# Kernel optimization log

Hardware: AMD Instinct MI355X
Metric: run time of the kernel (lower is better)

## Reference

```python
import jax, jax.numpy as jnp
import numpy as np

SHIFT_MIN, SHIFT_MAX = -14.0, 0.0  # deepshift range for weight_bits=5: (-(2**4-2), 0)


def shift_quant(w):
    """Quantize weights to signed powers of two (bit-shift weights), STE form."""
    sign = jnp.sign(w)
    shift = jnp.clip(jnp.round(jnp.log2(jnp.abs(w) + 1e-12)), SHIFT_MIN, SHIFT_MAX)
    q = sign * jnp.exp2(shift)
    return w + jax.lax.stop_gradient(q - w)


def moe_fc(t, wg, w0, b0, w1, b1):
    """Top-1 routing over 2 experts: expert0 dense Linear, expert1 shift-quantized Linear.
    t: [T, C]; weights torch-layout [out, in]. With top_k=1 the softmaxed top-k gate is 1.0,
    so combine is a hard select of the chosen expert's output."""
    logits = t @ wg                      # [T, 2]
    pick0 = (jnp.argmax(logits, axis=-1) == 0)[:, None]
    y0 = t @ w0.T + b0                   # dense expert
    y1 = t @ shift_quant(w1).T + b1      # shift expert
    return jnp.where(pick0, y0, y1)


def setup_inputs() -> dict:
    key = jax.random.key(0)
    ks = jax.random.split(key, 10)
    B, N, C, Dh = 16, 1024, 512, 2048
    s = 0.02
    return {
        "x": jax.random.normal(ks[0], (B, N, C), jnp.float32),
        "H": 32,
        "W": 32,
        "wg1": jax.random.normal(ks[1], (C, 2), jnp.float32) * s,
        "fc1_w0": jax.random.normal(ks[2], (Dh, C), jnp.float32) * s,
        "fc1_b0": jnp.zeros((Dh,), jnp.float32),
        "fc1_w1": jax.random.normal(ks[3], (Dh, C), jnp.float32) * s,
        "fc1_b1": jnp.zeros((Dh,), jnp.float32),
        "dw_w": jax.random.normal(ks[4], (Dh, 1, 3, 3), jnp.float32) * np.sqrt(2.0 / 9.0),
        "dw_b": jnp.zeros((Dh,), jnp.float32),
        "wg2": jax.random.normal(ks[5], (Dh, 2), jnp.float32) * s,
        "fc2_w0": jax.random.normal(ks[6], (C, Dh), jnp.float32) * s,
        "fc2_b0": jnp.zeros((C,), jnp.float32),
        "fc2_w1": jax.random.normal(ks[7], (C, Dh), jnp.float32) * s,
        "fc2_b1": jnp.zeros((C,), jnp.float32),
    }


def reference(x, H, W, wg1, fc1_w0, fc1_b0, fc1_w1, fc1_b1, dw_w, dw_b,
              wg2, fc2_w0, fc2_b0, fc2_w1, fc2_b1):
    B, N, C = x.shape
    Dh = fc1_w0.shape[0]
    # fc1 MoE
    h = moe_fc(x.reshape(-1, C), wg1, fc1_w0, fc1_b0, fc1_w1, fc1_b1)  # [B*N, Dh]
    # DWConv 3x3 depthwise, NCHW
    h = h.reshape(B, N, Dh).transpose(0, 2, 1).reshape(B, Dh, H, W)
    h = jax.lax.conv_general_dilated(
        h, dw_w, window_strides=(1, 1), padding="SAME",
        dimension_numbers=("NCHW", "OIHW", "NCHW"), feature_group_count=Dh)
    h = h + dw_b[None, :, None, None]
    h = h.reshape(B, Dh, N).transpose(0, 2, 1)  # [B, N, Dh]
    # GELU (exact, as nn.GELU default); dropout p=0 -> identity
    h = jax.nn.gelu(h, approximate=False)
    # fc2 MoE
    y = moe_fc(h.reshape(-1, Dh), wg2, fc2_w0, fc2_b0, fc2_w1, fc2_b1)
    return y.reshape(B, N, -1)
```

## Files before the change

### kernel.cpp

```cpp
#include <hip/hip_runtime.h>
#include <hip/hip_bf16.h>


#define TOKS  16384
#define CIN   512
#define DHID  2048

typedef __attribute__((ext_vector_type(8))) __bf16 bf16x8;
typedef __attribute__((ext_vector_type(4))) float  f32x4;
typedef __attribute__((ext_vector_type(4))) float  float4v;
typedef __attribute__((ext_vector_type(4))) unsigned short ushort4v;

__device__ __forceinline__ unsigned short f2bf(float f) {
  union { float f; unsigned int u; } a; a.f = f;
  unsigned int u = a.u;
  unsigned int r = u + 0x7FFFu + ((u >> 16) & 1u);
  return (unsigned short)(r >> 16);
}
__device__ __forceinline__ float bf2f(unsigned short h) {
  union { unsigned int u; float f; } a; a.u = ((unsigned int)h) << 16;
  return a.f;
}

__device__ __forceinline__ float squant(float w) {
  if (w == 0.0f) return 0.0f;
  float aw = fabsf(w) + 1e-12f;
  union { float f; unsigned u; } a; a.f = aw;
  int e = (int)((a.u >> 23) & 0xFFu) - 127;
  unsigned frac = a.u & 0x7FFFFFu;
  int shift = e + (frac >= 0x3504F4u ? 1 : 0);
  shift = min(max(shift, -14), 0);
  union { unsigned u; float f; } q; q.u = (unsigned)(shift + 127) << 23;
  return (w > 0.0f) ? q.f : -q.f;
}

#define GLDS16(gp, lp) __builtin_amdgcn_global_load_lds(                      \
    (const __attribute__((address_space(1))) void*)(gp),                      \
    (__attribute__((address_space(3))) void*)(lp), 16, 0, 0)

__global__ void k_prep(const float* __restrict__ w0, const float* __restrict__ w1,
                       const float* __restrict__ w20, const float* __restrict__ w21,
                       unsigned short* __restrict__ w0hi, unsigned short* __restrict__ w0lo,
                       unsigned short* __restrict__ w1q, unsigned short* __restrict__ w20b,
                       unsigned short* __restrict__ w21b) {
  int i = blockIdx.x * 256 + threadIdx.x;
  if (i >= DHID * CIN) return;
  float v = w0[i];
  unsigned short h = f2bf(v);
  w0hi[i] = h;
  w0lo[i] = f2bf(v - bf2f(h));
  w1q[i]  = f2bf(squant(w1[i]));
  w20b[i] = f2bf(w20[i]);
  w21b[i] = f2bf(squant(w21[i]));
}

__global__ void k_prepx(const float* __restrict__ x,
                        unsigned short* __restrict__ xhi, unsigned short* __restrict__ xlo) {
  int i = blockIdx.x * 256 + threadIdx.x;
  float4v v = ((const float4v*)x)[i];
  ushort4v hv, lv;
  #pragma unroll
  for (int q = 0; q < 4; ++q) {
    unsigned short h = f2bf(v[q]);
    hv[q] = h;
    lv[q] = f2bf(v[q] - bf2f(h));
  }
  ((ushort4v*)xhi)[i] = hv;
  ((ushort4v*)xlo)[i] = lv;
}

__global__ void k_gate1(const float* __restrict__ x, const float* __restrict__ wg1,
                        unsigned char* __restrict__ pick1) {
  int tok = blockIdx.x * 4 + (threadIdx.x >> 6);
  int l = threadIdx.x & 63;
  const float* xr = x + (size_t)tok * CIN;
  float s0 = 0.f, s1 = 0.f;
  for (int i = l; i < CIN; i += 64) {
    float v = xr[i];
    s0 += v * wg1[i * 2 + 0];
    s1 += v * wg1[i * 2 + 1];
  }
  for (int m = 32; m; m >>= 1) { s0 += __shfl_xor(s0, m); s1 += __shfl_xor(s1, m); }
  if (l == 0) pick1[tok] = (s0 >= s1) ? 0 : 1;
}

__global__ void k_scan(const unsigned char* __restrict__ pick, int* __restrict__ perm,
                       int* __restrict__ n0buf) {
  __shared__ int cnt[1024];
  const int t = threadIdx.x;
  unsigned char loc[16];
  int c0 = 0;
  #pragma unroll
  for (int i = 0; i < 16; ++i) { loc[i] = pick[t * 16 + i]; c0 += (loc[i] == 0); }
  cnt[t] = c0;
  __syncthreads();
  for (int off = 1; off < 1024; off <<= 1) {
    int v = cnt[t] + ((t >= off) ? cnt[t - off] : 0);
    __syncthreads();
    cnt[t] = v;
    __syncthreads();
  }
  int total0 = cnt[1023];
  int pre0 = cnt[t] - c0;
  int pre1 = t * 16 - pre0;
  if (t == 0) n0buf[0] = total0;
  int p0 = pre0, p1 = total0 + pre1;
  #pragma unroll
  for (int i = 0; i < 16; ++i) {
    int tok = t * 16 + i;
    if (loc[i] == 0) perm[p0++] = tok; else perm[p1++] = tok;
  }
}

__launch_bounds__(256, 2)
__global__ void k_fc1(const unsigned short* __restrict__ xhi,
                      const unsigned short* __restrict__ xlo,
                      const unsigned short* __restrict__ w0hi,
                      const unsigned short* __restrict__ w0lo,
                      const unsigned short* __restrict__ w1q,
                      const float* __restrict__ b0, const float* __restrict__ b1,
                      const int* __restrict__ perm, const int* __restrict__ n0buf,
                      float* __restrict__ h32) {
  __shared__ unsigned short sm[40960];
  const int t = threadIdx.x, wv = t >> 6, ln = t & 63;
  const int lr = ln & 15, lg = ln >> 4;
  const int g = blockIdx.x, q = g >> 3;
  const int tok0 = ((g & 7) + ((q >> 4) << 3)) * 128;
  const int nbase = (q & 15) * 128;
  const int wm = (wv >> 1) * 64, wn = (wv & 1) * 64;
  const int n0 = n0buf[0];
  const bool do0 = (tok0 < n0), do1 = (tok0 + 128 > n0);

  int par[2];
  #pragma unroll
  for (int s = 0; s < 2; ++s)
    par[s] = perm[tok0 + ((s * 4 + wv) << 4) + (ln >> 2)];

  const int swsrc = (((ln & 3) ^ ((ln >> 3) & 3)) << 3);
  const int swrd  = ((lg ^ ((lr >> 1) & 3)) << 3);

  f32x4 acc0[4][4], acc1[4][4];
  #pragma unroll
  for (int i = 0; i < 4; ++i)
    #pragma unroll
    for (int j = 0; j < 4; ++j) {
      acc0[i][j] = f32x4{0.f, 0.f, 0.f, 0.f};
      acc1[i][j] = f32x4{0.f, 0.f, 0.f, 0.f};
    }

  auto STAGE = [&](int kt, int db) {
    const int k0 = kt * 32;
    #pragma unroll
    for (int s = 0; s < 2; ++s) {
      const int rowblk = s * 4 + wv;
      const int aoff = db * 8192 + (rowblk << 9);
      const int boff = 16384 + db * 12288 + (rowblk << 9);
      size_t ga = (size_t)par[s] * CIN + k0 + swsrc;
      size_t gb = (size_t)(nbase + (rowblk << 4) + (ln >> 2)) * CIN + k0 + swsrc;
      GLDS16(xhi + ga, &sm[aoff]);
      GLDS16(xlo + ga, &sm[aoff + 4096]);
      GLDS16(w0hi + gb, &sm[boff]);
      GLDS16(w0lo + gb, &sm[boff + 4096]);
      GLDS16(w1q + gb, &sm[boff + 8192]);
    }
  };

  auto COMPUTE = [&](int db) {
    bf16x8 ah[4], al[4];
    #pragma unroll
    for (int mt = 0; mt < 4; ++mt) {
      int ro = (wm + (mt << 4) + lr) * 32 + swrd;
      ah[mt] = *(const bf16x8*)&sm[db * 8192 + ro];
      al[mt] = *(const bf16x8*)&sm[db * 8192 + 4096 + ro];
    }
    __builtin_amdgcn_s_setprio(1);
    #pragma unroll
    for (int nt = 0; nt < 4; ++nt) {
      int bb = 16384 + db * 12288 + (wn + (nt << 4) + lr) * 32 + swrd;
      if (do0) {
        bf16x8 bh = *(const bf16x8*)&sm[bb];
        bf16x8 bl = *(const bf16x8*)&sm[bb + 4096];
        #pragma unroll
        for (int mt = 0; mt < 4; ++mt) {
          acc0[mt][nt] = __builtin_amdgcn_mfma_f32_16x16x32_bf16(ah[mt], bh, acc0[mt][nt], 0, 0, 0);
          acc0[mt][nt] = __builtin_amdgcn_mfma_f32_16x16x32_bf16(al[mt], bh, acc0[mt][nt], 0, 0, 0);
          acc0[mt][nt] = __builtin_amdgcn_mfma_f32_16x16x32_bf16(ah[mt], bl, acc0[mt][nt], 0, 0, 0);
        }
      }
      if (do1) {
        bf16x8 bq = *(const bf16x8*)&sm[bb + 8192];
        #pragma unroll
        for (int mt = 0; mt < 4; ++mt) {
          acc1[mt][nt] = __builtin_amdgcn_mfma_f32_16x16x32_bf16(ah[mt], bq, acc1[mt][nt], 0, 0, 0);
          acc1[mt][nt] = __builtin_amdgcn_mfma_f32_16x16x32_bf16(al[mt], bq, acc1[mt][nt], 0, 0, 0);
        }
      }
    }
    __builtin_amdgcn_s_setprio(0);
  };

  STAGE(0, 0);
  #pragma unroll 2
  for (int kt = 0; kt < 15; ++kt) {
    __builtin_amdgcn_s_barrier();
    __builtin_amdgcn_sched_barrier(0);
    STAGE(kt + 1, (kt + 1) & 1);
    asm volatile("s_waitcnt vmcnt(10)" ::: "memory");
    __builtin_amdgcn_s_barrier();
    __builtin_amdgcn_sched_barrier(0);
    COMPUTE(kt & 1);
  }
  asm volatile("s_waitcnt vmcnt(0)" ::: "memory");
  __builtin_amdgcn_s_barrier();
  __builtin_amdgcn_sched_barrier(0);
  COMPUTE(1);

  __syncthreads();
  float* smf = (float*)sm;
  float bi0[4], bi1[4];
  #pragma unroll
  for (int nt = 0; nt < 4; ++nt) {
    int d = nbase + wn + (nt << 4) + lr;
    bi0[nt] = b0[d]; bi1[nt] = b1[d];
  }
  #pragma unroll
  for (int mt = 0; mt < 4; ++mt) {
    #pragma unroll
    for (int nt = 0; nt < 4; ++nt) {
      f32x4 v0 = acc0[mt][nt], v1 = acc1[mt][nt];
      #pragma unroll
      for (int rr = 0; rr < 4; ++rr) {
        int pos = tok0 + wm + (mt << 4) + (lg << 2) + rr;
        float val = (pos >= n0) ? (v1[rr] + bi1[nt]) : (v0[rr] + bi0[nt]);
        smf[wv * 1088 + ((lg << 2) + rr) * 68 + (nt << 4) + lr] = val;
      }
    }
    #pragma unroll
    for (int p = 0; p < 4; ++p) {
      int row = (p << 2) + (ln >> 4);
      f32x4 vv = *(const f32x4*)&smf[wv * 1088 + row * 68 + ((ln & 15) << 2)];
      int tok = perm[tok0 + wm + (mt << 4) + row];
      *(f32x4*)&h32[(size_t)tok * DHID + nbase + wn + ((ln & 15) << 2)] = vv;
    }
  }
}

__launch_bounds__(256)
__global__ void k_conv(const float* __restrict__ h32, const float* __restrict__ dww,
                       const float* __restrict__ dwb, const float* __restrict__ wg2,
                       unsigned short* __restrict__ hb, float* __restrict__ part) {
  __shared__ float4v tile[10][32][8];
  const int dc = blockIdx.x;
  const int ys = blockIdx.y;
  const int b  = blockIdx.z;
  const int t = threadIdx.x;
  const int d0 = dc * 32, y0 = ys * 8;
  const int dl4 = t & 7, xq = t >> 3;

  #pragma unroll
  for (int ry = 0; ry < 10; ++ry) {
    int y = y0 - 1 + ry;
    float4v v = {0.f, 0.f, 0.f, 0.f};
    if (y >= 0 && y < 32)
      v = *(const float4v*)&h32[(size_t)(b * 1024 + y * 32 + xq) * DHID + d0 + dl4 * 4];
    tile[ry][xq][dl4] = v;
  }
  __syncthreads();

  const int d = d0 + dl4 * 4;
  float4v kk[9];
  #pragma unroll
  for (int i = 0; i < 9; ++i) {
    kk[i][0] = dww[(d + 0) * 9 + i]; kk[i][1] = dww[(d + 1) * 9 + i];
    kk[i][2] = dww[(d + 2) * 9 + i]; kk[i][3] = dww[(d + 3) * 9 + i];
  }
  const float4v bias = *(const float4v*)&dwb[d];
  float4v g0v, g1v;
  #pragma unroll
  for (int j = 0; j < 4; ++j) { g0v[j] = wg2[(d + j) * 2]; g1v[j] = wg2[(d + j) * 2 + 1]; }

  #pragma unroll
  for (int yy = 0; yy < 8; ++yy) {
    float4v s = bias;
    #pragma unroll
    for (int dy = 0; dy < 3; ++dy)
      #pragma unroll
      for (int dx = 0; dx < 3; ++dx) {
        int xs = xq + dx - 1;
        if (xs >= 0 && xs < 32) {
          float4v v = tile[yy + dy][xs][dl4];
          float4v k = kk[dy * 3 + dx];
          s[0] += v[0] * k[0]; s[1] += v[1] * k[1];
          s[2] += v[2] * k[2]; s[3] += v[3] * k[3];
        }
      }
    float4v gg;
    #pragma unroll
    for (int j = 0; j < 4; ++j)
      gg[j] = 0.5f * s[j] * (1.0f + erff(s[j] * 0.70710678118654752f));
    int tok = b * 1024 + (y0 + yy) * 32 + xq;
    ushort4v hv;
    #pragma unroll
    for (int j = 0; j < 4; ++j) hv[j] = f2bf(gg[j]);
    *(ushort4v*)&hb[(size_t)tok * DHID + d] = hv;
    float p0 = gg[0] * g0v[0] + gg[1] * g0v[1] + gg[2] * g0v[2] + gg[3] * g0v[3];
    float p1 = gg[0] * g1v[0] + gg[1] * g1v[1] + gg[2] * g1v[2] + gg[3] * g1v[3];
    p0 += __shfl_xor(p0, 1); p0 += __shfl_xor(p0, 2); p0 += __shfl_xor(p0, 4);
    p1 += __shfl_xor(p1, 1); p1 += __shfl_xor(p1, 2); p1 += __shfl_xor(p1, 4);
    if (dl4 == 0) {
      part[(size_t)tok * 128 + dc] = p0;
      part[(size_t)tok * 128 + 64 + dc] = p1;
    }
  }
}

__global__ void k_gate2(const float* __restrict__ part, unsigned char* __restrict__ pick2) {
  int tok = blockIdx.x * 4 + (threadIdx.x >> 6);
  int l = threadIdx.x & 63;
  const float* pr = part + (size_t)tok * 128;
  float s0 = pr[l], s1 = pr[64 + l];
  for (int m = 32; m; m >>= 1) { s0 += __shfl_xor(s0, m); s1 += __shfl_xor(s1, m); }
  if (l == 0) pick2[tok] = (s0 >= s1) ? 0 : 1;
}

__launch_bounds__(256, 2)
__global__ void k_fc2(const unsigned short* __restrict__ hb,
                      const unsigned short* __restrict__ w20b,
                      const unsigned short* __restrict__ w21b,
                      const float* __restrict__ b0, const float* __restrict__ b1,
                      const int* __restrict__ perm, const int* __restrict__ n0buf,
                      float* __restrict__ out) {
  __shared__ unsigned short sm[24576];
  const int t = threadIdx.x, wv = t >> 6, ln = t & 63;
  const int lr = ln & 15, lg = ln >> 4;
  const int g = blockIdx.x, q = g >> 3;
  const int tok0 = ((g & 7) + ((q >> 2) << 3)) * 128;
  const int nbase = (q & 3) * 128;
  const int wm = (wv >> 1) * 64, wn = (wv & 1) * 64;
  const int n0 = n0buf[0];
  const bool do0 = (tok0 < n0), do1 = (tok0 + 128 > n0);

  int par[2];
  #pragma unroll
  for (int s = 0; s < 2; ++s)
    par[s] = perm[tok0 + ((s * 4 + wv) << 4) + (ln >> 2)];

  const int swsrc = (((ln & 3) ^ ((ln >> 3) & 3)) << 3);
  const int swrd  = ((lg ^ ((lr >> 1) & 3)) << 3);

  f32x4 acc0[4][4], acc1[4][4];
  #pragma unroll
  for (int i = 0; i < 4; ++i)
    #pragma unroll
    for (int j = 0; j < 4; ++j) {
      acc0[i][j] = f32x4{0.f, 0.f, 0.f, 0.f};
      acc1[i][j] = f32x4{0.f, 0.f, 0.f, 0.f};
    }

  auto STAGE = [&](int kt, int db) {
    const int k0 = kt * 32;
    #pragma unroll
    for (int s = 0; s < 2; ++s) {
      const int rowblk = s * 4 + wv;
      const int aoff = db * 4096 + (rowblk << 9);
      const int boff = 8192 + db * 8192 + (rowblk << 9);
      size_t ga = (size_t)par[s] * DHID + k0 + swsrc;
      size_t gb = (size_t)(nbase + (rowblk << 4) + (ln >> 2)) * DHID + k0 + swsrc;
      GLDS16(hb + ga, &sm[aoff]);
      GLDS16(w20b + gb, &sm[boff]);
      GLDS16(w21b + gb, &sm[boff + 4096]);
    }
  };

  auto COMPUTE = [&](int db) {
    bf16x8 a[4];
    #pragma unroll
    for (int mt = 0; mt < 4; ++mt)
      a[mt] = *(const bf16x8*)&sm[db * 4096 + (wm + (mt << 4) + lr) * 32 + swrd];
    __builtin_amdgcn_s_setprio(1);
    #pragma unroll
    for (int nt = 0; nt < 4; ++nt) {
      int bb = 8192 + db * 8192 + (wn + (nt << 4) + lr) * 32 + swrd;
      if (do0) {
        bf16x8 b0f = *(const bf16x8*)&sm[bb];
        #pragma unroll
        for (int mt = 0; mt < 4; ++mt)
          acc0[mt][nt] = __builtin_amdgcn_mfma_f32_16x16x32_bf16(a[mt], b0f, acc0[mt][nt], 0, 0, 0);
      }
      if (do1) {
        bf16x8 b1f = *(const bf16x8*)&sm[bb + 4096];
        #pragma unroll
        for (int mt = 0; mt < 4; ++mt)
          acc1[mt][nt] = __builtin_amdgcn_mfma_f32_16x16x32_bf16(a[mt], b1f, acc1[mt][nt], 0, 0, 0);
      }
    }
    __builtin_amdgcn_s_setprio(0);
  };

  STAGE(0, 0);
  #pragma unroll 2
  for (int kt = 0; kt < 63; ++kt) {
    __builtin_amdgcn_s_barrier();
    __builtin_amdgcn_sched_barrier(0);
    STAGE(kt + 1, (kt + 1) & 1);
    asm volatile("s_waitcnt vmcnt(6)" ::: "memory");
    __builtin_amdgcn_s_barrier();
    __builtin_amdgcn_sched_barrier(0);
    COMPUTE(kt & 1);
  }
  asm volatile("s_waitcnt vmcnt(0)" ::: "memory");
  __builtin_amdgcn_s_barrier();
  __builtin_amdgcn_sched_barrier(0);
  COMPUTE(1);

  __syncthreads();
  float* smf = (float*)sm;
  float bi0[4], bi1[4];
  #pragma unroll
  for (int nt = 0; nt < 4; ++nt) {
    int c = nbase + wn + (nt << 4) + lr;
    bi0[nt] = b0[c]; bi1[nt] = b1[c];
  }
  #pragma unroll
  for (int mt = 0; mt < 4; ++mt) {
    #pragma unroll
    for (int nt = 0; nt < 4; ++nt) {
      f32x4 v0 = acc0[mt][nt], v1 = acc1[mt][nt];
      #pragma unroll
      for (int rr = 0; rr < 4; ++rr) {
        int pos = tok0 + wm + (mt << 4) + (lg << 2) + rr;
        float val = (pos >= n0) ? (v1[rr] + bi1[nt]) : (v0[rr] + bi0[nt]);
        smf[wv * 1088 + ((lg << 2) + rr) * 68 + (nt << 4) + lr] = val;
      }
    }
    #pragma unroll
    for (int p = 0; p < 4; ++p) {
      int row = (p << 2) + (ln >> 4);
      f32x4 vv = *(const f32x4*)&smf[wv * 1088 + row * 68 + ((ln & 15) << 2)];
      int tok = perm[tok0 + wm + (mt << 4) + row];
      *(f32x4*)&out[(size_t)tok * CIN + nbase + wn + ((ln & 15) << 2)] = vv;
    }
  }
}

extern "C" void kernel_launch(void* const* d_in, const int* in_sizes, int n_in,
                              void* d_out, int out_size, void* d_ws, size_t ws_size,
                              hipStream_t stream) {
  (void)in_sizes; (void)n_in; (void)out_size; (void)ws_size;
  const float* x   = (const float*)d_in[0];
  const float* wg1 = (const float*)d_in[3];
  const float* w0  = (const float*)d_in[4];
  const float* b0  = (const float*)d_in[5];
  const float* w1  = (const float*)d_in[6];
  const float* b1  = (const float*)d_in[7];
  const float* dww = (const float*)d_in[8];
  const float* dwb = (const float*)d_in[9];
  const float* wg2 = (const float*)d_in[10];
  const float* w20 = (const float*)d_in[11];
  const float* b20 = (const float*)d_in[12];
  const float* w21 = (const float*)d_in[13];
  const float* b21 = (const float*)d_in[14];
  float* out = (float*)d_out;

  char* ws = (char*)d_ws;
  const size_t MB2 = 1u << 21;
  unsigned short* w0hi = (unsigned short*)(ws + 0 * MB2);
  unsigned short* w0lo = (unsigned short*)(ws + 1 * MB2);
  unsigned short* w1q  = (unsigned short*)(ws + 2 * MB2);
  unsigned short* w20b = (unsigned short*)(ws + 3 * MB2);
  unsigned short* w21b = (unsigned short*)(ws + 4 * MB2);
  char* p = ws + 5 * MB2;
  unsigned short* xhi = (unsigned short*)p;            p += (size_t)TOKS * CIN * 2;
  unsigned short* xlo = (unsigned short*)p;            p += (size_t)TOKS * CIN * 2;
  unsigned char* pick1 = (unsigned char*)p;            p += 65536;
  unsigned char* pick2 = (unsigned char*)p;            p += 65536;
  int* perm1 = (int*)p;                                p += TOKS * 4;
  int* perm2 = (int*)p;                                p += TOKS * 4;
  int* n0a   = (int*)p;                                p += 256;
  int* n0b   = (int*)p;                                p += 256;
  float* part = (float*)p;                             p += (size_t)TOKS * 128 * 4;
  float* h32  = (float*)p;                             p += (size_t)TOKS * DHID * 4;
  unsigned short* hb = (unsigned short*)p;

  k_prep <<<4096, 256, 0, stream>>>(w0, w1, w20, w21, w0hi, w0lo, w1q, w20b, w21b);
  k_prepx<<<8192, 256, 0, stream>>>(x, xhi, xlo);
  k_gate1<<<4096, 256, 0, stream>>>(x, wg1, pick1);
  k_scan <<<1, 1024, 0, stream>>>(pick1, perm1, n0a);
  k_fc1  <<<2048, 256, 0, stream>>>(xhi, xlo, w0hi, w0lo, w1q, b0, b1, perm1, n0a, h32);
  k_conv <<<dim3(64, 4, 16), 256, 0, stream>>>(h32, dww, dwb, wg2, hb, part);
  k_gate2<<<4096, 256, 0, stream>>>(part, pick2);
  k_scan <<<1, 1024, 0, stream>>>(pick2, perm2, n0b);
  k_fc2  <<<512, 256, 0, stream>>>(hb, w20b, w21b, b20, b21, perm2, n0b, out);
}
```

Baseline: 424.6 us.

## Split MoE GEMMs per expert, load A directly to registers, triple-buffer B

Fuses the x bf16 split with the first gate into one kernel and replaces the scan's LDS Hillis-Steele loop with a wave shuffle scan. Each fc1/fc2 GEMM is split into two per-expert kernels. Blocks that hold no rows for their expert exit early, so the kernel stays uniform and needs fewer registers and less LDS. In the GEMMs the gathered activation rows now load straight from global memory into registers, and only the weights go through a three-stage LDS ring. fc2 now takes K=64 per stage. Boundary tiles that mix both experts now run in two kernels, which adds launches and reads the activations twice.

```diff
diff --git a/kernel.cpp b/kernel.cpp
--- a/kernel.cpp
+++ b/kernel.cpp
@@ -10,6 +10,7 @@
 typedef __attribute__((ext_vector_type(4))) float  f32x4;
 typedef __attribute__((ext_vector_type(4))) float  float4v;
 typedef __attribute__((ext_vector_type(4))) unsigned short ushort4v;
+typedef __attribute__((ext_vector_type(8))) unsigned short ushort8;
 
 __device__ __forceinline__ unsigned short f2bf(float f) {
   union { float f; unsigned int u; } a; a.f = f;
@@ -37,6 +38,9 @@
 #define GLDS16(gp, lp) __builtin_amdgcn_global_load_lds(                      \
     (const __attribute__((address_space(1))) void*)(gp),                      \
     (__attribute__((address_space(3))) void*)(lp), 16, 0, 0)
+
+#define SBAR()  { __builtin_amdgcn_s_barrier(); __builtin_amdgcn_sched_barrier(0); }
+#define VMCNT(n) asm volatile("s_waitcnt vmcnt(" #n ")" ::: "memory")
 
 __global__ void k_prep(const float* __restrict__ w0, const float* __restrict__ w1,
                        const float* __restrict__ w20, const float* __restrict__ w21,
@@ -54,56 +58,62 @@
   w21b[i] = f2bf(squant(w21[i]));
 }
 
-__global__ void k_prepx(const float* __restrict__ x,
-                        unsigned short* __restrict__ xhi, unsigned short* __restrict__ xlo) {
-  int i = blockIdx.x * 256 + threadIdx.x;
-  float4v v = ((const float4v*)x)[i];
-  ushort4v hv, lv;
-  #pragma unroll
-  for (int q = 0; q < 4; ++q) {
-    unsigned short h = f2bf(v[q]);
-    hv[q] = h;
-    lv[q] = f2bf(v[q] - bf2f(h));
-  }
-  ((ushort4v*)xhi)[i] = hv;
-  ((ushort4v*)xlo)[i] = lv;
-}
-
-__global__ void k_gate1(const float* __restrict__ x, const float* __restrict__ wg1,
+__global__ void k_prepg(const float* __restrict__ x, const float* __restrict__ wg1,
+                        unsigned short* __restrict__ xhi, unsigned short* __restrict__ xlo,
                         unsigned char* __restrict__ pick1) {
-  int tok = blockIdx.x * 4 + (threadIdx.x >> 6);
-  int l = threadIdx.x & 63;
-  const float* xr = x + (size_t)tok * CIN;
+  __shared__ float wg[1024];
+  const int t = threadIdx.x;
+  #pragma unroll
+  for (int i = 0; i < 4; ++i) wg[t + i * 256] = wg1[t + i * 256];
+  __syncthreads();
+  const int tok = blockIdx.x * 4 + (t >> 6);
+  const int l = t & 63;
+  const float* xr = x + (size_t)tok * CIN + l * 8;
+  float4v v0 = *(const float4v*)xr;
+  float4v v1 = *(const float4v*)(xr + 4);
   float s0 = 0.f, s1 = 0.f;
-  for (int i = l; i < CIN; i += 64) {
-    float v = xr[i];
-    s0 += v * wg1[i * 2 + 0];
-    s1 += v * wg1[i * 2 + 1];
-  }
+  ushort8 hv, lv;
+  #pragma unroll
+  for (int j = 0; j < 8; ++j) {
+    float v = (j < 4) ? v0[j] : v1[j - 4];
+    unsigned short h = f2bf(v);
+    hv[j] = h;
+    lv[j] = f2bf(v - bf2f(h));
+    int c = l * 8 + j;
+    s0 += v * wg[c * 2];
+    s1 += v * wg[c * 2 + 1];
+  }
+  *(ushort8*)&xhi[(size_t)tok * CIN + l * 8] = hv;
+  *(ushort8*)&xlo[(size_t)tok * CIN + l * 8] = lv;
   for (int m = 32; m; m >>= 1) { s0 += __shfl_xor(s0, m); s1 += __shfl_xor(s1, m); }
   if (l == 0) pick1[tok] = (s0 >= s1) ? 0 : 1;
 }
 
 __global__ void k_scan(const unsigned char* __restrict__ pick, int* __restrict__ perm,
                        int* __restrict__ n0buf) {
-  __shared__ int cnt[1024];
+  __shared__ int wpre[17];
   const int t = threadIdx.x;
-  unsigned char loc[16];
-  int c0 = 0;
+  const int lane = t & 63, w = t >> 6;
+  unsigned char loc[16]; int c0 = 0;
   #pragma unroll
   for (int i = 0; i < 16; ++i) { loc[i] = pick[t * 16 + i]; c0 += (loc[i] == 0); }
-  cnt[t] = c0;
+  int s = c0;
+  #pragma unroll
+  for (int off = 1; off < 64; off <<= 1) {
+    int v = __shfl_up(s, off);
+    if (lane >= off) s += v;
+  }
+  if (lane == 63) wpre[w + 1] = s;
+  if (t == 0) wpre[0] = 0;
   __syncthreads();
-  for (int off = 1; off < 1024; off <<= 1) {
-    int v = cnt[t] + ((t >= off) ? cnt[t - off] : 0);
-    __syncthreads();
-    cnt[t] = v;
-    __syncthreads();
-  }
-  int total0 = cnt[1023];
-  int pre0 = cnt[t] - c0;
+  if (t == 0) {
+    for (int j = 1; j <= 16; ++j) wpre[j] += wpre[j - 1];
+    n0buf[0] = wpre[16];
+  }
+  __syncthreads();
+  int total0 = wpre[16];
+  int pre0 = wpre[w] + s - c0;
   int pre1 = t * 16 - pre0;
-  if (t == 0) n0buf[0] = total0;
   int p0 = pre0, p1 = total0 + pre1;
   #pragma unroll
   for (int i = 0; i < 16; ++i) {
@@ -113,134 +123,238 @@
 }
 
 __launch_bounds__(256, 2)
-__global__ void k_fc1(const unsigned short* __restrict__ xhi,
-                      const unsigned short* __restrict__ xlo,
-                      const unsigned short* __restrict__ w0hi,
-                      const unsigned short* __restrict__ w0lo,
-                      const unsigned short* __restrict__ w1q,
-                      const float* __restrict__ b0, const float* __restrict__ b1,
-                      const int* __restrict__ perm, const int* __restrict__ n0buf,
-                      float* __restrict__ h32) {
-  __shared__ unsigned short sm[40960];
+__global__ void k_fc1_e0(const unsigned short* __restrict__ xhi,
+                         const unsigned short* __restrict__ xlo,
+                         const unsigned short* __restrict__ w0hi,
+                         const unsigned short* __restrict__ w0lo,
+                         const float* __restrict__ b0,
+                         const int* __restrict__ perm, const int* __restrict__ n0buf,
+                         float* __restrict__ h32) {
+  __shared__ unsigned short sm[24576];
+  const int n0 = n0buf[0];
   const int t = threadIdx.x, wv = t >> 6, ln = t & 63;
   const int lr = ln & 15, lg = ln >> 4;
   const int g = blockIdx.x, q = g >> 3;
   const int tok0 = ((g & 7) + ((q >> 4) << 3)) * 128;
   const int nbase = (q & 15) * 128;
+  if (tok0 >= n0) return;
   const int wm = (wv >> 1) * 64, wn = (wv & 1) * 64;
-  const int n0 = n0buf[0];
-  const bool do0 = (tok0 < n0), do1 = (tok0 + 128 > n0);
-
-  int par[2];
-  #pragma unroll
-  for (int s = 0; s < 2; ++s)
-    par[s] = perm[tok0 + ((s * 4 + wv) << 4) + (ln >> 2)];
+
+  int rowoff[4];
+  #pragma unroll
+  for (int mt = 0; mt < 4; ++mt)
+    rowoff[mt] = perm[tok0 + wm + (mt << 4) + lr] * CIN + (lg << 3);
 
   const int swsrc = (((ln & 3) ^ ((ln >> 3) & 3)) << 3);
   const int swrd  = ((lg ^ ((lr >> 1) & 3)) << 3);
 
-  f32x4 acc0[4][4], acc1[4][4];
+  f32x4 acc[4][4];
   #pragma unroll
   for (int i = 0; i < 4; ++i)
     #pragma unroll
-    for (int j = 0; j < 4; ++j) {
-      acc0[i][j] = f32x4{0.f, 0.f, 0.f, 0.f};
-      acc1[i][j] = f32x4{0.f, 0.f, 0.f, 0.f};
-    }
-
-  auto STAGE = [&](int kt, int db) {
+    for (int j = 0; j < 4; ++j) acc[i][j] = f32x4{0.f, 0.f, 0.f, 0.f};
+
+  auto STAGEB = [&](int kt, int db) {
     const int k0 = kt * 32;
     #pragma unroll
     for (int s = 0; s < 2; ++s) {
       const int rowblk = s * 4 + wv;
-      const int aoff = db * 8192 + (rowblk << 9);
-      const int boff = 16384 + db * 12288 + (rowblk << 9);
-      size_t ga = (size_t)par[s] * CIN + k0 + swsrc;
       size_t gb = (size_t)(nbase + (rowblk << 4) + (ln >> 2)) * CIN + k0 + swsrc;
-      GLDS16(xhi + ga, &sm[aoff]);
-      GLDS16(xlo + ga, &sm[aoff + 4096]);
-      GLDS16(w0hi + gb, &sm[boff]);
-      GLDS16(w0lo + gb, &sm[boff + 4096]);
-      GLDS16(w1q + gb, &sm[boff + 8192]);
-    }
-  };
-
-  auto COMPUTE = [&](int db) {
-    bf16x8 ah[4], al[4];
+      GLDS16(w0hi + gb, &sm[db * 8192 + (rowblk << 9)]);
+      GLDS16(w0lo + gb, &sm[db * 8192 + 4096 + (rowblk << 9)]);
+    }
+  };
+  auto LOADA = [&](bf16x8 (&ah)[4], bf16x8 (&al)[4], int kt) {
+    const int k0 = kt * 32;
     #pragma unroll
     for (int mt = 0; mt < 4; ++mt) {
-      int ro = (wm + (mt << 4) + lr) * 32 + swrd;
-      ah[mt] = *(const bf16x8*)&sm[db * 8192 + ro];
-      al[mt] = *(const bf16x8*)&sm[db * 8192 + 4096 + ro];
-    }
+      ah[mt] = *(const bf16x8*)&xhi[rowoff[mt] + k0];
+      al[mt] = *(const bf16x8*)&xlo[rowoff[mt] + k0];
+    }
+  };
+  auto COMPUTE = [&](const bf16x8 (&ah)[4], const bf16x8 (&al)[4], int db) {
     __builtin_amdgcn_s_setprio(1);
     #pragma unroll
     for (int nt = 0; nt < 4; ++nt) {
-      int bb = 16384 + db * 12288 + (wn + (nt << 4) + lr) * 32 + swrd;
-      if (do0) {
-        bf16x8 bh = *(const bf16x8*)&sm[bb];
-        bf16x8 bl = *(const bf16x8*)&sm[bb + 4096];
-        #pragma unroll
-        for (int mt = 0; mt < 4; ++mt) {
-          acc0[mt][nt] = __builtin_amdgcn_mfma_f32_16x16x32_bf16(ah[mt], bh, acc0[mt][nt], 0, 0, 0);
-          acc0[mt][nt] = __builtin_amdgcn_mfma_f32_16x16x32_bf16(al[mt], bh, acc0[mt][nt], 0, 0, 0);
-          acc0[mt][nt] = __builtin_amdgcn_mfma_f32_16x16x32_bf16(ah[mt], bl, acc0[mt][nt], 0, 0, 0);
-        }
-      }
-      if (do1) {
-        bf16x8 bq = *(const bf16x8*)&sm[bb + 8192];
-        #pragma unroll
-        for (int mt = 0; mt < 4; ++mt) {
-          acc1[mt][nt] = __builtin_amdgcn_mfma_f32_16x16x32_bf16(ah[mt], bq, acc1[mt][nt], 0, 0, 0);
-          acc1[mt][nt] = __builtin_amdgcn_mfma_f32_16x16x32_bf16(al[mt], bq, acc1[mt][nt], 0, 0, 0);
-        }
+      int bb = db * 8192 + (wn + (nt << 4) + lr) * 32 + swrd;
+      bf16x8 bh = *(const bf16x8*)&sm[bb];
+      bf16x8 bl = *(const bf16x8*)&sm[bb + 4096];
+      #pragma unroll
+      for (int mt = 0; mt < 4; ++mt) {
+        acc[mt][nt] = __builtin_amdgcn_mfma_f32_16x16x32_bf16(ah[mt], bh, acc[mt][nt], 0, 0, 0);
+        acc[mt][nt] = __builtin_amdgcn_mfma_f32_16x16x32_bf16(al[mt], bh, acc[mt][nt], 0, 0, 0);
+        acc[mt][nt] = __builtin_amdgcn_mfma_f32_16x16x32_bf16(ah[mt], bl, acc[mt][nt], 0, 0, 0);
       }
     }
     __builtin_amdgcn_s_setprio(0);
   };
 
-  STAGE(0, 0);
-  #pragma unroll 2
-  for (int kt = 0; kt < 15; ++kt) {
-    __builtin_amdgcn_s_barrier();
-    __builtin_amdgcn_sched_barrier(0);
-    STAGE(kt + 1, (kt + 1) & 1);
-    asm volatile("s_waitcnt vmcnt(10)" ::: "memory");
-    __builtin_amdgcn_s_barrier();
-    __builtin_amdgcn_sched_barrier(0);
-    COMPUTE(kt & 1);
-  }
-  asm volatile("s_waitcnt vmcnt(0)" ::: "memory");
-  __builtin_amdgcn_s_barrier();
-  __builtin_amdgcn_sched_barrier(0);
-  COMPUTE(1);
+  bf16x8 Ah0[4], Al0[4], Ah1[4], Al1[4];
+  LOADA(Ah0, Al0, 0);
+  STAGEB(0, 0);
+  STAGEB(1, 1);
+  for (int kt = 0; kt < 14; kt += 2) {
+    SBAR();
+    LOADA(Ah1, Al1, kt + 1);
+    STAGEB(kt + 2, (kt + 2) % 3);
+    VMCNT(16);
+    SBAR();
+    COMPUTE(Ah0, Al0, kt % 3);
+    SBAR();
+    LOADA(Ah0, Al0, kt + 2);
+    STAGEB(kt + 3, (kt + 3) % 3);
+    VMCNT(16);
+    SBAR();
+    COMPUTE(Ah1, Al1, (kt + 1) % 3);
+  }
+  SBAR();
+  LOADA(Ah1, Al1, 15);
+  VMCNT(12);
+  SBAR();
+  COMPUTE(Ah0, Al0, 2);
+  SBAR();
+  VMCNT(0);
+  SBAR();
+  COMPUTE(Ah1, Al1, 0);
 
   __syncthreads();
   float* smf = (float*)sm;
-  float bi0[4], bi1[4];
-  #pragma unroll
-  for (int nt = 0; nt < 4; ++nt) {
-    int d = nbase + wn + (nt << 4) + lr;
-    bi0[nt] = b0[d]; bi1[nt] = b1[d];
-  }
+  float bi[4];
+  #pragma unroll
+  for (int nt = 0; nt < 4; ++nt) bi[nt] = b0[nbase + wn + (nt << 4) + lr];
   #pragma unroll
   for (int mt = 0; mt < 4; ++mt) {
     #pragma unroll
     for (int nt = 0; nt < 4; ++nt) {
-      f32x4 v0 = acc0[mt][nt], v1 = acc1[mt][nt];
-      #pragma unroll
-      for (int rr = 0; rr < 4; ++rr) {
-        int pos = tok0 + wm + (mt << 4) + (lg << 2) + rr;
-        float val = (pos >= n0) ? (v1[rr] + bi1[nt]) : (v0[rr] + bi0[nt]);
-        smf[wv * 1088 + ((lg << 2) + rr) * 68 + (nt << 4) + lr] = val;
-      }
+      f32x4 v = acc[mt][nt];
+      #pragma unroll
+      for (int rr = 0; rr < 4; ++rr)
+        smf[wv * 1088 + ((lg << 2) + rr) * 68 + (nt << 4) + lr] = v[rr] + bi[nt];
     }
     #pragma unroll
     for (int p = 0; p < 4; ++p) {
       int row = (p << 2) + (ln >> 4);
-      f32x4 vv = *(const f32x4*)&smf[wv * 1088 + row * 68 + ((ln & 15) << 2)];
-      int tok = perm[tok0 + wm + (mt << 4) + row];
-      *(f32x4*)&h32[(size_t)tok * DHID + nbase + wn + ((ln & 15) << 2)] = vv;
+      int pos = tok0 + wm + (mt << 4) + row;
+      if (pos < n0) {
+        f32x4 vv = *(const f32x4*)&smf[wv * 1088 + row * 68 + ((ln & 15) << 2)];
+        *(f32x4*)&h32[(size_t)perm[pos] * DHID + nbase + wn + ((ln & 15) << 2)] = vv;
+      }
+    }
+  }
+}
+
+__launch_bounds__(256, 2)
+__global__ void k_fc1_e1(const unsigned short* __restrict__ xhi,
+                         const unsigned short* __restrict__ xlo,
+                         const unsigned short* __restrict__ w1q,
+                         const float* __restrict__ b1,
+                         const int* __restrict__ perm, const int* __restrict__ n0buf,
+                         float* __restrict__ h32) {
+  __shared__ unsigned short sm[12288];
+  const int n0 = n0buf[0];
+  const int t = threadIdx.x, wv = t >> 6, ln = t & 63;
+  const int lr = ln & 15, lg = ln >> 4;
+  const int g = blockIdx.x, q = g >> 3;
+  const int tok0 = ((g & 7) + ((q >> 4) << 3)) * 128;
+  const int nbase = (q & 15) * 128;
+  if (tok0 + 128 <= n0) return;
+  const int wm = (wv >> 1) * 64, wn = (wv & 1) * 64;
+
+  int rowoff[4];
+  #pragma unroll
+  for (int mt = 0; mt < 4; ++mt)
+    rowoff[mt] = perm[tok0 + wm + (mt << 4) + lr] * CIN + (lg << 3);
+
+  const int swsrc = (((ln & 3) ^ ((ln >> 3) & 3)) << 3);
+  const int swrd  = ((lg ^ ((lr >> 1) & 3)) << 3);
+
+  f32x4 acc[4][4];
+  #pragma unroll
+  for (int i = 0; i < 4; ++i)
+    #pragma unroll
+    for (int j = 0; j < 4; ++j) acc[i][j] = f32x4{0.f, 0.f, 0.f, 0.f};
+
+  auto STAGEB = [&](int kt, int db) {
+    const int k0 = kt * 32;
+    #pragma unroll
+    for (int s = 0; s < 2; ++s) {
+      const int rowblk = s * 4 + wv;
+      size_t gb = (size_t)(nbase + (rowblk << 4) + (ln >> 2)) * CIN + k0 + swsrc;
+      GLDS16(w1q + gb, &sm[db * 4096 + (rowblk << 9)]);
+    }
+  };
+  auto LOADA = [&](bf16x8 (&ah)[4], bf16x8 (&al)[4], int kt) {
+    const int k0 = kt * 32;
+    #pragma unroll
+    for (int mt = 0; mt < 4; ++mt) {
+      ah[mt] = *(const bf16x8*)&xhi[rowoff[mt] + k0];
+      al[mt] = *(const bf16x8*)&xlo[rowoff[mt] + k0];
+    }
+  };
+  auto COMPUTE = [&](const bf16x8 (&ah)[4], const bf16x8 (&al)[4], int db) {
+    __builtin_amdgcn_s_setprio(1);
+    #pragma unroll
+    for (int nt = 0; nt < 4; ++nt) {
+      bf16x8 bq = *(const bf16x8*)&sm[db * 4096 + (wn + (nt << 4) + lr) * 32 + swrd];
+      #pragma unroll
+      for (int mt = 0; mt < 4; ++mt) {
+        acc[mt][nt] = __builtin_amdgcn_mfma_f32_16x16x32_bf16(ah[mt], bq, acc[mt][nt], 0, 0, 0);
+        acc[mt][nt] = __builtin_amdgcn_mfma_f32_16x16x32_bf16(al[mt], bq, acc[mt][nt], 0, 0, 0);
+      }
+    }
+    __builtin_amdgcn_s_setprio(0);
+  };
+
+  bf16x8 Ah0[4], Al0[4], Ah1[4], Al1[4];
+  LOADA(Ah0, Al0, 0);
+  STAGEB(0, 0);
+  STAGEB(1, 1);
+  for (int kt = 0; kt < 14; kt += 2) {
+    SBAR();
+    LOADA(Ah1, Al1, kt + 1);
+    STAGEB(kt + 2, (kt + 2) % 3);
+    VMCNT(12);
+    SBAR();
+    COMPUTE(Ah0, Al0, kt % 3);
+    SBAR();
+    LOADA(Ah0, Al0, kt + 2);
+    STAGEB(kt + 3, (kt + 3) % 3);
+    VMCNT(12);
+    SBAR();
+    COMPUTE(Ah1, Al1, (kt + 1) % 3);
+  }
+  SBAR();
+  LOADA(Ah1, Al1, 15);
+  VMCNT(10);
+  SBAR();
+  COMPUTE(Ah0, Al0, 2);
+  SBAR();
+  VMCNT(0);
+  SBAR();
+  COMPUTE(Ah1, Al1, 0);
+
+  __syncthreads();
+  float* smf = (float*)sm;
+  float bi[4];
+  #pragma unroll
+  for (int nt = 0; nt < 4; ++nt) bi[nt] = b1[nbase + wn + (nt << 4) + lr];
+  #pragma unroll
+  for (int mt = 0; mt < 4; ++mt) {
+    #pragma unroll
+    for (int nt = 0; nt < 4; ++nt) {
+      f32x4 v = acc[mt][nt];
+      #pragma unroll
+      for (int rr = 0; rr < 4; ++rr)
+        smf[wv * 1088 + ((lg << 2) + rr) * 68 + (nt << 4) + lr] = v[rr] + bi[nt];
+    }
+    #pragma unroll
+    for (int p = 0; p < 4; ++p) {
+      int row = (p << 2) + (ln >> 4);
+      int pos = tok0 + wm + (mt << 4) + row;
+      if (pos >= n0) {
+        f32x4 vv = *(const f32x4*)&smf[wv * 1088 + row * 68 + ((ln & 15) << 2)];
+        *(f32x4*)&h32[(size_t)perm[pos] * DHID + nbase + wn + ((ln & 15) << 2)] = vv;
+      }
     }
   }
 }
@@ -323,122 +437,125 @@
   if (l == 0) pick2[tok] = (s0 >= s1) ? 0 : 1;
 }
 
+template <int EXPERT>
 __launch_bounds__(256, 2)
-__global__ void k_fc2(const unsigned short* __restrict__ hb,
-                      const unsigned short* __restrict__ w20b,
-                      const unsigned short* __restrict__ w21b,
-                      const float* __restrict__ b0, const float* __restrict__ b1,
-                      const int* __restrict__ perm, const int* __restrict__ n0buf,
-                      float* __restrict__ out) {
+__global__ void k_fc2_e(const unsigned short* __restrict__ hb,
+                        const unsigned short* __restrict__ wb,
+                        const float* __restrict__ bias_v,
+                        const int* __restrict__ perm, const int* __restrict__ n0buf,
+                        float* __restrict__ out) {
   __shared__ unsigned short sm[24576];
+  const int n0 = n0buf[0];
   const int t = threadIdx.x, wv = t >> 6, ln = t & 63;
   const int lr = ln & 15, lg = ln >> 4;
   const int g = blockIdx.x, q = g >> 3;
   const int tok0 = ((g & 7) + ((q >> 2) << 3)) * 128;
   const int nbase = (q & 3) * 128;
+  if (EXPERT == 0) { if (tok0 >= n0) return; }
+  else             { if (tok0 + 128 <= n0) return; }
   const int wm = (wv >> 1) * 64, wn = (wv & 1) * 64;
-  const int n0 = n0buf[0];
-  const bool do0 = (tok0 < n0), do1 = (tok0 + 128 > n0);
-
-  int par[2];
-  #pragma unroll
-  for (int s = 0; s < 2; ++s)
-    par[s] = perm[tok0 + ((s * 4 + wv) << 4) + (ln >> 2)];
+
+  int rowoff[4];
+  #pragma unroll
+  for (int mt = 0; mt < 4; ++mt)
+    rowoff[mt] = perm[tok0 + wm + (mt << 4) + lr] * DHID + (lg << 3);
 
   const int swsrc = (((ln & 3) ^ ((ln >> 3) & 3)) << 3);
   const int swrd  = ((lg ^ ((lr >> 1) & 3)) << 3);
 
-  f32x4 acc0[4][4], acc1[4][4];
+  f32x4 acc[4][4];
   #pragma unroll
   for (int i = 0; i < 4; ++i)
     #pragma unroll
-    for (int j = 0; j < 4; ++j) {
-      acc0[i][j] = f32x4{0.f, 0.f, 0.f, 0.f};
-      acc1[i][j] = f32x4{0.f, 0.f, 0.f, 0.f};
-    }
-
-  auto STAGE = [&](int kt, int db) {
-    const int k0 = kt * 32;
-    #pragma unroll
-    for (int s = 0; s < 2; ++s) {
-      const int rowblk = s * 4 + wv;
-      const int aoff = db * 4096 + (rowblk << 9);
-      const int boff = 8192 + db * 8192 + (rowblk << 9);
-      size_t ga = (size_t)par[s] * DHID + k0 + swsrc;
-      size_t gb = (size_t)(nbase + (rowblk << 4) + (ln >> 2)) * DHID + k0 + swsrc;
-      GLDS16(hb + ga, &sm[aoff]);
-      GLDS16(w20b + gb, &sm[boff]);
-      GLDS16(w21b + gb, &sm[boff + 4096]);
-    }
-  };
-
-  auto COMPUTE = [&](int db) {
-    bf16x8 a[4];
-    #pragma unroll
-    for (int mt = 0; mt < 4; ++mt)
-      a[mt] = *(const bf16x8*)&sm[db * 4096 + (wm + (mt << 4) + lr) * 32 + swrd];
+    for (int j = 0; j < 4; ++j) acc[i][j] = f32x4{0.f, 0.f, 0.f, 0.f};
+
+  auto STAGEB = [&](int kt, int db) {
+    #pragma unroll
+    for (int ks = 0; ks < 2; ++ks) {
+      const int k0 = kt * 64 + ks * 32;
+      #pragma unroll
+      for (int s = 0; s < 2; ++s) {
+        const int rowblk = s * 4 + wv;
+        size_t gb = (size_t)(nbase + (rowblk << 4) + (ln >> 2)) * DHID + k0 + swsrc;
+        GLDS16(wb + gb, &sm[db * 8192 + ks * 4096 + (rowblk << 9)]);
+      }
+    }
+  };
+  auto LOADA = [&](bf16x8 (&a)[8], int kt) {
+    #pragma unroll
+    for (int ks = 0; ks < 2; ++ks) {
+      const int k0 = kt * 64 + ks * 32;
+      #pragma unroll
+      for (int mt = 0; mt < 4; ++mt)
+        a[ks * 4 + mt] = *(const bf16x8*)&hb[rowoff[mt] + k0];
+    }
+  };
+  auto COMPUTE = [&](const bf16x8 (&a)[8], int db) {
     __builtin_amdgcn_s_setprio(1);
     #pragma unroll
-    for (int nt = 0; nt < 4; ++nt) {
-      int bb = 8192 + db * 8192 + (wn + (nt << 4) + lr) * 32 + swrd;
-      if (do0) {
-        bf16x8 b0f = *(const bf16x8*)&sm[bb];
+    for (int ks = 0; ks < 2; ++ks) {
+      #pragma unroll
+      for (int nt = 0; nt < 4; ++nt) {
+        bf16x8 bf = *(const bf16x8*)&sm[db * 8192 + ks * 4096 + (wn + (nt << 4) + lr) * 32 + swrd];
         #pragma unroll
         for (int mt = 0; mt < 4; ++mt)
-          acc0[mt][nt] = __builtin_amdgcn_mfma_f32_16x16x32_bf16(a[mt], b0f, acc0[mt][nt], 0, 0, 0);
-      }
-      if (do1) {
-        bf16x8 b1f = *(const bf16x8*)&sm[bb + 4096];
-        #pragma unroll
-        for (int mt = 0; mt < 4; ++mt)
-          acc1[mt][nt] = __builtin_amdgcn_mfma_f32_16x16x32_bf16(a[mt], b1f, acc1[mt][nt], 0, 0, 0);
+          acc[mt][nt] = __builtin_amdgcn_mfma_f32_16x16x32_bf16(a[ks * 4 + mt], bf, acc[mt][nt], 0, 0, 0);
       }
     }
     __builtin_amdgcn_s_setprio(0);
   };
 
-  STAGE(0, 0);
-  #pragma unroll 2
-  for (int kt = 0; kt < 63; ++kt) {
-    __builtin_amdgcn_s_barrier();
-    __builtin_amdgcn_sched_barrier(0);
-    STAGE(kt + 1, (kt + 1) & 1);
-    asm volatile("s_waitcnt vmcnt(6)" ::: "memory");
-    __builtin_amdgcn_s_barrier();
-    __builtin_amdgcn_sched_barrier(0);
-    COMPUTE(kt & 1);
-  }
-  asm volatile("s_waitcnt vmcnt(0)" ::: "memory");
-  __builtin_amdgcn_s_barrier();
-  __builtin_amdgcn_sched_barrier(0);
-  COMPUTE(1);
+  bf16x8 A0[8], A1[8];
+  LOADA(A0, 0);
+  STAGEB(0, 0);
+  STAGEB(1, 1);
+  for (int kt = 0; kt < 30; kt += 2) {
+    SBAR();
+    LOADA(A1, kt + 1);
+    STAGEB(kt + 2, (kt + 2) % 3);
+    VMCNT(16);
+    SBAR();
+    COMPUTE(A0, kt % 3);
+    SBAR();
+    LOADA(A0, kt + 2);
+    STAGEB(kt + 3, (kt + 3) % 3);
+    VMCNT(16);
+    SBAR();
+    COMPUTE(A1, (kt + 1) % 3);
+  }
+  SBAR();
+  LOADA(A1, 31);
+  VMCNT(12);
+  SBAR();
+  COMPUTE(A0, 0);
+  SBAR();
+  VMCNT(0);
+  SBAR();
+  COMPUTE(A1, 1);
 
   __syncthreads();
   float* smf = (float*)sm;
-  float bi0[4], bi1[4];
-  #pragma unroll
-  for (int nt = 0; nt < 4; ++nt) {
-    int c = nbase + wn + (nt << 4) + lr;
-    bi0[nt] = b0[c]; bi1[nt] = b1[c];
-  }
+  float bi[4];
+  #pragma unroll
+  for (int nt = 0; nt < 4; ++nt) bi[nt] = bias_v[nbase + wn + (nt << 4) + lr];
   #pragma unroll
   for (int mt = 0; mt < 4; ++mt) {
     #pragma unroll
     for (int nt = 0; nt < 4; ++nt) {
-      f32x4 v0 = acc0[mt][nt], v1 = acc1[mt][nt];
-      #pragma unroll
-      for (int rr = 0; rr < 4; ++rr) {
-        int pos = tok0 + wm + (mt << 4) + (lg << 2) + rr;
-        float val = (pos >= n0) ? (v1[rr] + bi1[nt]) : (v0[rr] + bi0[nt]);
-        smf[wv * 1088 + ((lg << 2) + rr) * 68 + (nt << 4) + lr] = val;
-      }
+      f32x4 v = acc[mt][nt];
+      #pragma unroll
+      for (int rr = 0; rr < 4; ++rr)
+        smf[wv * 1088 + ((lg << 2) + rr) * 68 + (nt << 4) + lr] = v[rr] + bi[nt];
     }
     #pragma unroll
     for (int p = 0; p < 4; ++p) {
       int row = (p << 2) + (ln >> 4);
-      f32x4 vv = *(const f32x4*)&smf[wv * 1088 + row * 68 + ((ln & 15) << 2)];
-      int tok = perm[tok0 + wm + (mt << 4) + row];
-      *(f32x4*)&out[(size_t)tok * CIN + nbase + wn + ((ln & 15) << 2)] = vv;
+      int pos = tok0 + wm + (mt << 4) + row;
+      bool store = (EXPERT == 0) ? (pos < n0) : (pos >= n0);
+      if (store) {
+        f32x4 vv = *(const f32x4*)&smf[wv * 1088 + row * 68 + ((ln & 15) << 2)];
+        *(f32x4*)&out[(size_t)perm[pos] * CIN + nbase + wn + ((ln & 15) << 2)] = vv;
+      }
     }
   }
 }
@@ -483,12 +600,13 @@
   unsigned short* hb = (unsigned short*)p;
 
   k_prep <<<4096, 256, 0, stream>>>(w0, w1, w20, w21, w0hi, w0lo, w1q, w20b, w21b);
-  k_prepx<<<8192, 256, 0, stream>>>(x, xhi, xlo);
-  k_gate1<<<4096, 256, 0, stream>>>(x, wg1, pick1);
+  k_prepg<<<4096, 256, 0, stream>>>(x, wg1, xhi, xlo, pick1);
   k_scan <<<1, 1024, 0, stream>>>(pick1, perm1, n0a);
-  k_fc1  <<<2048, 256, 0, stream>>>(xhi, xlo, w0hi, w0lo, w1q, b0, b1, perm1, n0a, h32);
+  k_fc1_e0<<<2048, 256, 0, stream>>>(xhi, xlo, w0hi, w0lo, b0, perm1, n0a, h32);
+  k_fc1_e1<<<2048, 256, 0, stream>>>(xhi, xlo, w1q, b1, perm1, n0a, h32);
   k_conv <<<dim3(64, 4, 16), 256, 0, stream>>>(h32, dww, dwb, wg2, hb, part);
   k_gate2<<<4096, 256, 0, stream>>>(part, pick2);
   k_scan <<<1, 1024, 0, stream>>>(pick2, perm2, n0b);
-  k_fc2  <<<512, 256, 0, stream>>>(hb, w20b, w21b, b20, b21, perm2, n0b, out);
-}
+  k_fc2_e<0><<<512, 256, 0, stream>>>(hb, w20b, b20, perm2, n0b, out);
+  k_fc2_e<1><<<512, 256, 0, stream>>>(hb, w21b, b21, perm2, n0b, out);
+}
```

After: 418.0 us. No clear change (-1.6%).
